# Performance work log

Hardware: AMD Instinct MI355X
Metric: run time of the kernel (lower is better)

The kernel has to match this reference:

```python
import jax, jax.numpy as jnp
import numpy as np

B, S, H, NH = 4, 4096, 1024, 16
D = H // NH
SCALE = 1.0 / float(np.sqrt(D))


def setup_inputs() -> dict:
    key = jax.random.key(0)
    ks = jax.random.split(key, 4)
    w = 0.02
    return {
        "hidden_states": jax.random.normal(ks[0], (B, S, H), jnp.float32),
        "attention_mask": jnp.zeros((B, 1, 1, S), jnp.float32),
        "Wq": jax.random.normal(ks[1], (H, H), jnp.float32) * w,
        "bq": jnp.zeros((H,), jnp.float32),
        "Wk": jax.random.normal(ks[2], (H, H), jnp.float32) * w,
        "bk": jnp.zeros((H,), jnp.float32),
        "Wv": jax.random.normal(ks[3], (H, H), jnp.float32) * w,
        "bv": jnp.zeros((H,), jnp.float32),
    }


def reference(hidden_states, attention_mask, Wq, bq, Wk, bk, Wv, bv):
    def heads(x):  # [B,S,H] -> [B,NH,S,D]
        return x.reshape(B, S, NH, D).transpose(0, 2, 1, 3)

    q = heads(hidden_states @ Wq.T + bq)
    k = heads(hidden_states @ Wk.T + bk)
    v = heads(hidden_states @ Wv.T + bv)

    # --- global token (position 0) attends to everything ---
    gq = q[:, :, 0:1]                                   # [B,NH,1,D]
    g_scores = jnp.einsum('bhqd,bhkd->bhqk', gq, k) * SCALE + attention_mask
    g_attn = jax.nn.softmax(g_scores, axis=-1)          # [B,NH,1,S]
    g_out = jnp.einsum('bhqk,bhkd->bhqd', g_attn, v)    # [B,NH,1,D]

    # --- local tokens: 2-way attention over {own key, global key} ---
    lq = q[:, :, 1:]                                    # [B,NH,S-1,D]
    s_self = jnp.einsum('bhsd,bhsd->bhs', lq, k[:, :, 1:]) * SCALE
    s_glob = jnp.einsum('bhsd,bhd->bhs', lq, k[:, :, 0]) * SCALE
    # order matches torch cat([own, global]) along the key axis
    l_attn = jax.nn.softmax(jnp.stack([s_self, s_glob], axis=-1), axis=-1)  # [B,NH,S-1,2]
    l_out = l_attn[..., 0:1] * v[:, :, 1:] + l_attn[..., 1:2] * v[:, :, 0:1]  # [B,NH,S-1,D]

    ctx = jnp.concatenate([g_out, l_out], axis=2)       # [B,NH,S,D]
    ctx = ctx.transpose(0, 2, 1, 3).reshape(B, S, H)
    # torch returns local_attentions with shape [B,NH,S-1,1,2]
    return ctx, l_attn[:, :, :, None, :]
```

## Files before the change

### kernel.cpp

```cpp
#include <hip/hip_runtime.h>
#include <cstdint>
#include <cstddef>

#define B_   4
#define S_   4096
#define H_   1024
#define NH_  16
#define D_   64
#define M_TOT (B_ * S_)
#define K_TOT H_
#define N_TOT (3 * H_)
#define SCALE_ 0.125f
#define NCH 4
#define CH (S_ / NCH)

typedef __bf16 bf16x8 __attribute__((ext_vector_type(8)));
typedef float  f32x4  __attribute__((ext_vector_type(4)));

__device__ __forceinline__ unsigned short f2b(float x) {
    unsigned int u = __float_as_uint(x);
    u += 0x7FFFu + ((u >> 16) & 1u);
    return (unsigned short)(u >> 16);
}
__device__ __forceinline__ float b2f(unsigned int u) {
    return __uint_as_float(u << 16);
}

__global__ __launch_bounds__(256) void cvt_x(const float* __restrict__ src,
                                             unsigned short* __restrict__ dst, int n4) {
    int i = blockIdx.x * blockDim.x + threadIdx.x;
    int stride = gridDim.x * blockDim.x;
    for (; i < n4; i += stride) {
        float4 v = ((const float4*)src)[i];
        ushort4 o;
        o.x = f2b(v.x); o.y = f2b(v.y); o.z = f2b(v.z); o.w = f2b(v.w);
        ((ushort4*)dst)[i] = o;
    }
}

__global__ __launch_bounds__(256) void cvt_w(const float* __restrict__ w0,
                                             const float* __restrict__ w1,
                                             const float* __restrict__ w2,
                                             unsigned short* __restrict__ dst) {
    const int per4 = H_ * H_ / 4;
    int i = blockIdx.x * blockDim.x + threadIdx.x;
    const float* s = (blockIdx.y == 0) ? w0 : (blockIdx.y == 1 ? w1 : w2);
    float4 v = ((const float4*)s)[i];
    ushort4 o;
    o.x = f2b(v.x); o.y = f2b(v.y); o.z = f2b(v.z); o.w = f2b(v.w);
    ((ushort4*)(dst + (size_t)blockIdx.y * H_ * H_))[i] = o;
}

__global__ __launch_bounds__(256) void gemm_qkv(const unsigned short* __restrict__ A,
                                                const unsigned short* __restrict__ W,
                                                const float* __restrict__ bq,
                                                const float* __restrict__ bk,
                                                const float* __restrict__ bv,
                                                unsigned short* __restrict__ C) {
    __shared__ unsigned short As[128 * 32] __attribute__((aligned(16)));
    __shared__ unsigned short Bs[128 * 32] __attribute__((aligned(16)));
    const int tid  = threadIdx.x;
    const int wid  = tid >> 6;
    const int lane = tid & 63;
    const int wm = wid >> 1, wn = wid & 1;
    const int m0 = blockIdx.y * 128;
    const int n0 = blockIdx.x * 128;

    f32x4 acc[4][4];
#pragma unroll
    for (int i = 0; i < 4; i++)
#pragma unroll
        for (int j = 0; j < 4; j++) acc[i][j] = (f32x4){0.f, 0.f, 0.f, 0.f};

    const int lrow = lane >> 2;
    const int lcol = (lane & 3) * 8;

    for (int k0 = 0; k0 < K_TOT; k0 += 32) {
#pragma unroll
        for (int i = 0; i < 2; i++) {
            const int r0 = wid * 32 + i * 16;
            const unsigned short* ga = A + (size_t)(m0 + r0 + lrow) * K_TOT + k0 + lcol;
            __builtin_amdgcn_global_load_lds(
                (const __attribute__((address_space(1))) void*)ga,
                (__attribute__((address_space(3))) void*)&As[r0 * 32], 16, 0, 0);
            const unsigned short* gb = W + (size_t)(n0 + r0 + lrow) * K_TOT + k0 + lcol;
            __builtin_amdgcn_global_load_lds(
                (const __attribute__((address_space(1))) void*)gb,
                (__attribute__((address_space(3))) void*)&Bs[r0 * 32], 16, 0, 0);
        }
        __syncthreads();

        bf16x8 af[4], bfv[4];
#pragma unroll
        for (int mi = 0; mi < 4; mi++)
            af[mi] = *(const bf16x8*)&As[(wm * 64 + mi * 16 + (lane & 15)) * 32 + (lane >> 4) * 8];
#pragma unroll
        for (int ni = 0; ni < 4; ni++)
            bfv[ni] = *(const bf16x8*)&Bs[(wn * 64 + ni * 16 + (lane & 15)) * 32 + (lane >> 4) * 8];
#pragma unroll
        for (int mi = 0; mi < 4; mi++)
#pragma unroll
            for (int ni = 0; ni < 4; ni++)
                acc[mi][ni] = __builtin_amdgcn_mfma_f32_16x16x32_bf16(af[mi], bfv[ni], acc[mi][ni], 0, 0, 0);
        __syncthreads();
    }

    const int col_l = lane & 15;
    const int quad  = lane >> 4;
#pragma unroll
    for (int mi = 0; mi < 4; mi++) {
#pragma unroll
        for (int ni = 0; ni < 4; ni++) {
            const int gc = n0 + wn * 64 + ni * 16 + col_l;
            const float bias = (gc < H_) ? bq[gc] : (gc < 2 * H_ ? bk[gc - H_] : bv[gc - 2 * H_]);
#pragma unroll
            for (int i = 0; i < 4; i++) {
                const int gr = m0 + wm * 64 + mi * 16 + quad * 4 + i;
                C[(size_t)gr * N_TOT + gc] = f2b(acc[mi][ni][i] + bias);
            }
        }
    }
}

__global__ __launch_bounds__(256) void gattn_part(const unsigned short* __restrict__ QKV,
                                                  const float* __restrict__ mask,
                                                  float* __restrict__ Pm,
                                                  float* __restrict__ Pl,
                                                  float* __restrict__ Po) {
    const int bh = blockIdx.x;
    const int b = bh >> 4, h = bh & 15;
    const int chunk = blockIdx.y;
    const int tid = threadIdx.x;
    const int w = tid >> 6, lane = tid & 63;

    __shared__ float gq_sh[D_];
    __shared__ float pr[CH];
    __shared__ float red[8];
    __shared__ float osum[4][D_];

    const unsigned short* gqp = QKV + (size_t)(b * S_) * N_TOT + h * D_;
    if (tid < D_) gq_sh[tid] = b2f(gqp[tid]);
    __syncthreads();

    const int s0 = chunk * CH;
    float sreg[4];
    float smax = -1e30f;
    for (int j = 0; j < 4; j++) {
        const int sl = tid + j * 256;
        const int s  = s0 + sl;
        const uint4* kp4 = (const uint4*)(QKV + (size_t)(b * S_ + s) * N_TOT + H_ + h * D_);
        float acc = 0.f;
#pragma unroll
        for (int c = 0; c < 8; c++) {
            uint4 r = kp4[c];
            acc += b2f(r.x & 0xffffu) * gq_sh[c * 8 + 0];
            acc += b2f(r.x >> 16)     * gq_sh[c * 8 + 1];
            acc += b2f(r.y & 0xffffu) * gq_sh[c * 8 + 2];
            acc += b2f(r.y >> 16)     * gq_sh[c * 8 + 3];
            acc += b2f(r.z & 0xffffu) * gq_sh[c * 8 + 4];
            acc += b2f(r.z >> 16)     * gq_sh[c * 8 + 5];
            acc += b2f(r.w & 0xffffu) * gq_sh[c * 8 + 6];
            acc += b2f(r.w >> 16)     * gq_sh[c * 8 + 7];
        }
        const float sv = acc * SCALE_ + mask[b * S_ + s];
        sreg[j] = sv;
        smax = fmaxf(smax, sv);
    }
    float wmax = smax;
#pragma unroll
    for (int m = 32; m >= 1; m >>= 1) wmax = fmaxf(wmax, __shfl_xor(wmax, m, 64));
    if (lane == 0) red[w] = wmax;
    __syncthreads();
    const float bmax = fmaxf(fmaxf(red[0], red[1]), fmaxf(red[2], red[3]));

    float lsum = 0.f;
    for (int j = 0; j < 4; j++) {
        const int sl = tid + j * 256;
        const float p = __expf(sreg[j] - bmax);
        pr[sl] = p;
        lsum += p;
    }
    float wsum = lsum;
#pragma unroll
    for (int m = 32; m >= 1; m >>= 1) wsum += __shfl_xor(wsum, m, 64);
    if (lane == 0) red[4 + w] = wsum;
    __syncthreads();
    const float bsum = red[4] + red[5] + red[6] + red[7];

    float o = 0.f;
    const int sbase = s0 + w * 256;
    for (int i = 0; i < 256; i++) {
        const int s = sbase + i;
        const float vv = b2f((unsigned int)QKV[(size_t)(b * S_ + s) * N_TOT + 2 * H_ + h * D_ + lane]);
        o += pr[w * 256 + i] * vv;
    }
    osum[w][lane] = o;
    __syncthreads();
    if (tid < D_) {
        const float ot = osum[0][tid] + osum[1][tid] + osum[2][tid] + osum[3][tid];
        Po[(size_t)(bh * NCH + chunk) * D_ + tid] = ot;
        if (tid == 0) {
            Pm[bh * NCH + chunk] = bmax;
            Pl[bh * NCH + chunk] = bsum;
        }
    }
}

__global__ __launch_bounds__(64) void gattn_comb(const float* __restrict__ Pm,
                                                 const float* __restrict__ Pl,
                                                 const float* __restrict__ Po,
                                                 float* __restrict__ out) {
    const int bh = blockIdx.x, d = threadIdx.x;
    const int b = bh >> 4, h = bh & 15;
    const float m0 = Pm[bh * 4 + 0], m1 = Pm[bh * 4 + 1], m2 = Pm[bh * 4 + 2], m3 = Pm[bh * 4 + 3];
    const float ms = fmaxf(fmaxf(m0, m1), fmaxf(m2, m3));
    const float e0 = __expf(m0 - ms), e1 = __expf(m1 - ms), e2 = __expf(m2 - ms), e3 = __expf(m3 - ms);
    const float z = Pl[bh * 4 + 0] * e0 + Pl[bh * 4 + 1] * e1 + Pl[bh * 4 + 2] * e2 + Pl[bh * 4 + 3] * e3;
    const float o = Po[(size_t)(bh * 4 + 0) * D_ + d] * e0 + Po[(size_t)(bh * 4 + 1) * D_ + d] * e1 +
                    Po[(size_t)(bh * 4 + 2) * D_ + d] * e2 + Po[(size_t)(bh * 4 + 3) * D_ + d] * e3;
    out[(size_t)b * S_ * H_ + (size_t)h * D_ + d] = o / z;
}

__global__ __launch_bounds__(256) void lattn(const unsigned short* __restrict__ QKV,
                                             float* __restrict__ ctx,
                                             float* __restrict__ lat) {
    const int bh = blockIdx.x;
    const int b = bh >> 4, h = bh & 15;
    const int w = threadIdx.x >> 6, lane = threadIdx.x & 63;
    const int s = 1 + blockIdx.y * 4 + w;
    if (s >= S_) return;

    const size_t rowS = (size_t)(b * S_ + s) * N_TOT + h * D_;
    const size_t row0 = (size_t)(b * S_) * N_TOT + h * D_;
    const float qd  = b2f((unsigned int)QKV[rowS + lane]);
    const float kd  = b2f((unsigned int)QKV[rowS + H_ + lane]);
    const float k0d = b2f((unsigned int)QKV[row0 + H_ + lane]);

    float ps = qd * kd, pg = qd * k0d;
#pragma unroll
    for (int m = 32; m >= 1; m >>= 1) {
        ps += __shfl_xor(ps, m, 64);
        pg += __shfl_xor(pg, m, 64);
    }
    ps *= SCALE_; pg *= SCALE_;
    const float mx = fmaxf(ps, pg);
    const float e0 = __expf(ps - mx), e1 = __expf(pg - mx);
    const float z = e0 + e1;
    const float p0 = e0 / z, p1 = e1 / z;

    const float vd  = b2f((unsigned int)QKV[rowS + 2 * H_ + lane]);
    const float v0d = b2f((unsigned int)QKV[row0 + 2 * H_ + lane]);
    ctx[(size_t)b * (S_ * H_) + (size_t)s * H_ + h * D_ + lane] = p0 * vd + p1 * v0d;
    if (lane == 0) {
        const size_t li = ((size_t)bh * (S_ - 1) + (s - 1)) * 2;
        lat[li]     = p0;
        lat[li + 1] = p1;
    }
}

extern "C" void kernel_launch(void* const* d_in, const int* in_sizes, int n_in,
                              void* d_out, int out_size, void* d_ws, size_t ws_size,
                              hipStream_t stream) {
    const float* hs   = (const float*)d_in[0];
    const float* mask = (const float*)d_in[1];
    const float* Wq   = (const float*)d_in[2];
    const float* bq   = (const float*)d_in[3];
    const float* Wk   = (const float*)d_in[4];
    const float* bk   = (const float*)d_in[5];
    const float* Wv   = (const float*)d_in[6];
    const float* bv   = (const float*)d_in[7];

    float* out = (float*)d_out;
    float* lat = out + (size_t)B_ * S_ * H_;

    char* ws = (char*)d_ws;
    const size_t offXb  = 0;
    const size_t offWb  = offXb  + (size_t)M_TOT * K_TOT * 2;
    const size_t offQKV = offWb  + (size_t)3 * H_ * H_ * 2;
    const size_t offPm  = offQKV + (size_t)M_TOT * N_TOT * 2;
    const size_t offPl  = offPm  + (size_t)B_ * NH_ * NCH * 4;
    const size_t offPo  = offPl  + (size_t)B_ * NH_ * NCH * 4;

    unsigned short* Xb  = (unsigned short*)(ws + offXb);
    unsigned short* Wb  = (unsigned short*)(ws + offWb);
    unsigned short* QKV = (unsigned short*)(ws + offQKV);
    float* Pm = (float*)(ws + offPm);
    float* Pl = (float*)(ws + offPl);
    float* Po = (float*)(ws + offPo);

    hipLaunchKernelGGL(cvt_x, dim3(4096), dim3(256), 0, stream, hs, Xb, M_TOT * K_TOT / 4);
    hipLaunchKernelGGL(cvt_w, dim3(H_ * H_ / 4 / 256, 3), dim3(256), 0, stream, Wq, Wk, Wv, Wb);
    hipLaunchKernelGGL(gemm_qkv, dim3(N_TOT / 128, M_TOT / 128), dim3(256), 0, stream,
                       Xb, Wb, bq, bk, bv, QKV);
    hipLaunchKernelGGL(gattn_part, dim3(B_ * NH_, NCH), dim3(256), 0, stream, QKV, mask, Pm, Pl, Po);
    hipLaunchKernelGGL(gattn_comb, dim3(B_ * NH_), dim3(64), 0, stream, Pm, Pl, Po, out);
    hipLaunchKernelGGL(lattn, dim3(B_ * NH_, 1024), dim3(256), 0, stream, QKV, out, lat);
}
```

Baseline: 346.2 us.

## Vectorize local attention, split global attention finer, merge conversion kernels

Fuses the input and weight bf16 conversion kernels into one launch. Increases the global-token attention split from 4 to 16 chunks so more blocks run with shorter serial V loops, and generalises the combine step accordingly. Rewrites local attention so each wave handles 8 rows with 16-byte vector loads and float4 stores instead of one row with scalar 2-byte accesses. This reduces launch overhead, improves occupancy and memory coalescing, at the cost of more partial results to combine.

```diff
diff --git a/kernel.cpp b/kernel.cpp
--- a/kernel.cpp
+++ b/kernel.cpp
@@ -11,7 +11,7 @@
 #define K_TOT H_
 #define N_TOT (3 * H_)
 #define SCALE_ 0.125f
-#define NCH 4
+#define NCH 16
 #define CH (S_ / NCH)
 
 typedef __bf16 bf16x8 __attribute__((ext_vector_type(8)));
@@ -25,30 +25,36 @@
 __device__ __forceinline__ float b2f(unsigned int u) {
     return __uint_as_float(u << 16);
 }
-
-__global__ __launch_bounds__(256) void cvt_x(const float* __restrict__ src,
-                                             unsigned short* __restrict__ dst, int n4) {
-    int i = blockIdx.x * blockDim.x + threadIdx.x;
-    int stride = gridDim.x * blockDim.x;
-    for (; i < n4; i += stride) {
-        float4 v = ((const float4*)src)[i];
-        ushort4 o;
+__device__ __forceinline__ void unp8(uint4 u, float* f) {
+    f[0] = b2f(u.x & 0xffffu); f[1] = b2f(u.x >> 16);
+    f[2] = b2f(u.y & 0xffffu); f[3] = b2f(u.y >> 16);
+    f[4] = b2f(u.z & 0xffffu); f[5] = b2f(u.z >> 16);
+    f[6] = b2f(u.w & 0xffffu); f[7] = b2f(u.w >> 16);
+}
+
+__global__ __launch_bounds__(256) void cvt_all(const float* __restrict__ hs,
+                                               const float* __restrict__ wq,
+                                               const float* __restrict__ wk,
+                                               const float* __restrict__ wv,
+                                               unsigned short* __restrict__ Xb,
+                                               unsigned short* __restrict__ Wb) {
+    const int i = blockIdx.x * 256 + threadIdx.x;
+    const int X4 = M_TOT * K_TOT / 4;
+    float4 v;
+    ushort4 o;
+    if (i < X4) {
+        v = ((const float4*)hs)[i];
         o.x = f2b(v.x); o.y = f2b(v.y); o.z = f2b(v.z); o.w = f2b(v.w);
-        ((ushort4*)dst)[i] = o;
-    }
-}
-
-__global__ __launch_bounds__(256) void cvt_w(const float* __restrict__ w0,
-                                             const float* __restrict__ w1,
-                                             const float* __restrict__ w2,
-                                             unsigned short* __restrict__ dst) {
-    const int per4 = H_ * H_ / 4;
-    int i = blockIdx.x * blockDim.x + threadIdx.x;
-    const float* s = (blockIdx.y == 0) ? w0 : (blockIdx.y == 1 ? w1 : w2);
-    float4 v = ((const float4*)s)[i];
-    ushort4 o;
-    o.x = f2b(v.x); o.y = f2b(v.y); o.z = f2b(v.z); o.w = f2b(v.w);
-    ((ushort4*)(dst + (size_t)blockIdx.y * H_ * H_))[i] = o;
+        ((ushort4*)Xb)[i] = o;
+    } else {
+        const int j = i - X4;
+        const int w = j >> 18;
+        const int off = j & 0x3ffff;
+        const float* s = (w == 0) ? wq : (w == 1 ? wk : wv);
+        v = ((const float4*)s)[off];
+        o.x = f2b(v.x); o.y = f2b(v.y); o.z = f2b(v.z); o.w = f2b(v.w);
+        ((ushort4*)(Wb + (size_t)w * H_ * H_))[off] = o;
+    }
 }
 
 __global__ __launch_bounds__(256) void gemm_qkv(const unsigned short* __restrict__ A,
@@ -143,44 +149,33 @@
     __syncthreads();
 
     const int s0 = chunk * CH;
-    float sreg[4];
-    float smax = -1e30f;
-    for (int j = 0; j < 4; j++) {
-        const int sl = tid + j * 256;
-        const int s  = s0 + sl;
-        const uint4* kp4 = (const uint4*)(QKV + (size_t)(b * S_ + s) * N_TOT + H_ + h * D_);
-        float acc = 0.f;
-#pragma unroll
-        for (int c = 0; c < 8; c++) {
-            uint4 r = kp4[c];
-            acc += b2f(r.x & 0xffffu) * gq_sh[c * 8 + 0];
-            acc += b2f(r.x >> 16)     * gq_sh[c * 8 + 1];
-            acc += b2f(r.y & 0xffffu) * gq_sh[c * 8 + 2];
-            acc += b2f(r.y >> 16)     * gq_sh[c * 8 + 3];
-            acc += b2f(r.z & 0xffffu) * gq_sh[c * 8 + 4];
-            acc += b2f(r.z >> 16)     * gq_sh[c * 8 + 5];
-            acc += b2f(r.w & 0xffffu) * gq_sh[c * 8 + 6];
-            acc += b2f(r.w >> 16)     * gq_sh[c * 8 + 7];
-        }
-        const float sv = acc * SCALE_ + mask[b * S_ + s];
-        sreg[j] = sv;
-        smax = fmaxf(smax, sv);
-    }
-    float wmax = smax;
+    const int s  = s0 + tid;
+    const uint4* kp4 = (const uint4*)(QKV + (size_t)(b * S_ + s) * N_TOT + H_ + h * D_);
+    float acc = 0.f;
+#pragma unroll
+    for (int c = 0; c < 8; c++) {
+        uint4 r = kp4[c];
+        acc += b2f(r.x & 0xffffu) * gq_sh[c * 8 + 0];
+        acc += b2f(r.x >> 16)     * gq_sh[c * 8 + 1];
+        acc += b2f(r.y & 0xffffu) * gq_sh[c * 8 + 2];
+        acc += b2f(r.y >> 16)     * gq_sh[c * 8 + 3];
+        acc += b2f(r.z & 0xffffu) * gq_sh[c * 8 + 4];
+        acc += b2f(r.z >> 16)     * gq_sh[c * 8 + 5];
+        acc += b2f(r.w & 0xffffu) * gq_sh[c * 8 + 6];
+        acc += b2f(r.w >> 16)     * gq_sh[c * 8 + 7];
+    }
+    const float sv = acc * SCALE_ + mask[b * S_ + s];
+
+    float wmax = sv;
 #pragma unroll
     for (int m = 32; m >= 1; m >>= 1) wmax = fmaxf(wmax, __shfl_xor(wmax, m, 64));
     if (lane == 0) red[w] = wmax;
     __syncthreads();
     const float bmax = fmaxf(fmaxf(red[0], red[1]), fmaxf(red[2], red[3]));
 
-    float lsum = 0.f;
-    for (int j = 0; j < 4; j++) {
-        const int sl = tid + j * 256;
-        const float p = __expf(sreg[j] - bmax);
-        pr[sl] = p;
-        lsum += p;
-    }
-    float wsum = lsum;
+    const float p = __expf(sv - bmax);
+    pr[tid] = p;
+    float wsum = p;
 #pragma unroll
     for (int m = 32; m >= 1; m >>= 1) wsum += __shfl_xor(wsum, m, 64);
     if (lane == 0) red[4 + w] = wsum;
@@ -188,11 +183,12 @@
     const float bsum = red[4] + red[5] + red[6] + red[7];
 
     float o = 0.f;
-    const int sbase = s0 + w * 256;
-    for (int i = 0; i < 256; i++) {
-        const int s = sbase + i;
-        const float vv = b2f((unsigned int)QKV[(size_t)(b * S_ + s) * N_TOT + 2 * H_ + h * D_ + lane]);
-        o += pr[w * 256 + i] * vv;
+    const int sbase = s0 + w * 64;
+#pragma unroll 8
+    for (int i = 0; i < 64; i++) {
+        const int si = sbase + i;
+        const float vv = b2f((unsigned int)QKV[(size_t)(b * S_ + si) * N_TOT + 2 * H_ + h * D_ + lane]);
+        o += pr[w * 64 + i] * vv;
     }
     osum[w][lane] = o;
     __syncthreads();
@@ -212,12 +208,16 @@
                                                  float* __restrict__ out) {
     const int bh = blockIdx.x, d = threadIdx.x;
     const int b = bh >> 4, h = bh & 15;
-    const float m0 = Pm[bh * 4 + 0], m1 = Pm[bh * 4 + 1], m2 = Pm[bh * 4 + 2], m3 = Pm[bh * 4 + 3];
-    const float ms = fmaxf(fmaxf(m0, m1), fmaxf(m2, m3));
-    const float e0 = __expf(m0 - ms), e1 = __expf(m1 - ms), e2 = __expf(m2 - ms), e3 = __expf(m3 - ms);
-    const float z = Pl[bh * 4 + 0] * e0 + Pl[bh * 4 + 1] * e1 + Pl[bh * 4 + 2] * e2 + Pl[bh * 4 + 3] * e3;
-    const float o = Po[(size_t)(bh * 4 + 0) * D_ + d] * e0 + Po[(size_t)(bh * 4 + 1) * D_ + d] * e1 +
-                    Po[(size_t)(bh * 4 + 2) * D_ + d] * e2 + Po[(size_t)(bh * 4 + 3) * D_ + d] * e3;
+    float ms = -1e30f;
+#pragma unroll
+    for (int c = 0; c < NCH; c++) ms = fmaxf(ms, Pm[bh * NCH + c]);
+    float z = 0.f, o = 0.f;
+#pragma unroll
+    for (int c = 0; c < NCH; c++) {
+        const float e = __expf(Pm[bh * NCH + c] - ms);
+        z += Pl[bh * NCH + c] * e;
+        o += Po[(size_t)(bh * NCH + c) * D_ + d] * e;
+    }
     out[(size_t)b * S_ * H_ + (size_t)h * D_ + d] = o / z;
 }
 
@@ -227,18 +227,25 @@
     const int bh = blockIdx.x;
     const int b = bh >> 4, h = bh & 15;
     const int w = threadIdx.x >> 6, lane = threadIdx.x & 63;
-    const int s = 1 + blockIdx.y * 4 + w;
+    const int g = lane >> 3;
+    const int l = lane & 7;
+    const int s = 1 + blockIdx.y * 32 + w * 8 + g;
     if (s >= S_) return;
 
-    const size_t rowS = (size_t)(b * S_ + s) * N_TOT + h * D_;
-    const size_t row0 = (size_t)(b * S_) * N_TOT + h * D_;
-    const float qd  = b2f((unsigned int)QKV[rowS + lane]);
-    const float kd  = b2f((unsigned int)QKV[rowS + H_ + lane]);
-    const float k0d = b2f((unsigned int)QKV[row0 + H_ + lane]);
-
-    float ps = qd * kd, pg = qd * k0d;
-#pragma unroll
-    for (int m = 32; m >= 1; m >>= 1) {
+    const size_t rowS = (size_t)(b * S_ + s) * N_TOT + h * D_ + l * 8;
+    const size_t row0 = (size_t)(b * S_) * N_TOT + h * D_ + l * 8;
+
+    uint4 qu  = *(const uint4*)(QKV + rowS);
+    uint4 ku  = *(const uint4*)(QKV + rowS + H_);
+    uint4 k0u = *(const uint4*)(QKV + row0 + H_);
+    float qf[8], kf[8], k0f[8];
+    unp8(qu, qf); unp8(ku, kf); unp8(k0u, k0f);
+
+    float ps = 0.f, pg = 0.f;
+#pragma unroll
+    for (int i = 0; i < 8; i++) { ps += qf[i] * kf[i]; pg += qf[i] * k0f[i]; }
+#pragma unroll
+    for (int m = 1; m < 8; m <<= 1) {
         ps += __shfl_xor(ps, m, 64);
         pg += __shfl_xor(pg, m, 64);
     }
@@ -248,13 +255,27 @@
     const float z = e0 + e1;
     const float p0 = e0 / z, p1 = e1 / z;
 
-    const float vd  = b2f((unsigned int)QKV[rowS + 2 * H_ + lane]);
-    const float v0d = b2f((unsigned int)QKV[row0 + 2 * H_ + lane]);
-    ctx[(size_t)b * (S_ * H_) + (size_t)s * H_ + h * D_ + lane] = p0 * vd + p1 * v0d;
-    if (lane == 0) {
-        const size_t li = ((size_t)bh * (S_ - 1) + (s - 1)) * 2;
-        lat[li]     = p0;
-        lat[li + 1] = p1;
+    uint4 vu  = *(const uint4*)(QKV + rowS + 2 * H_);
+    uint4 v0u = *(const uint4*)(QKV + row0 + 2 * H_);
+    float vf[8], v0f[8];
+    unp8(vu, vf); unp8(v0u, v0f);
+
+    float* cp = ctx + (size_t)b * (S_ * H_) + (size_t)s * H_ + h * D_ + l * 8;
+    float4 o0, o1;
+    o0.x = p0 * vf[0] + p1 * v0f[0];
+    o0.y = p0 * vf[1] + p1 * v0f[1];
+    o0.z = p0 * vf[2] + p1 * v0f[2];
+    o0.w = p0 * vf[3] + p1 * v0f[3];
+    o1.x = p0 * vf[4] + p1 * v0f[4];
+    o1.y = p0 * vf[5] + p1 * v0f[5];
+    o1.z = p0 * vf[6] + p1 * v0f[6];
+    o1.w = p0 * vf[7] + p1 * v0f[7];
+    ((float4*)cp)[0] = o0;
+    ((float4*)cp)[1] = o1;
+
+    if (l == 0) {
+        float2 lp; lp.x = p0; lp.y = p1;
+        ((float2*)(lat + ((size_t)bh * (S_ - 1) + (s - 1)) * 2))[0] = lp;
     }
 }
 
@@ -288,11 +309,12 @@
     float* Pl = (float*)(ws + offPl);
     float* Po = (float*)(ws + offPo);
 
-    hipLaunchKernelGGL(cvt_x, dim3(4096), dim3(256), 0, stream, hs, Xb, M_TOT * K_TOT / 4);
-    hipLaunchKernelGGL(cvt_w, dim3(H_ * H_ / 4 / 256, 3), dim3(256), 0, stream, Wq, Wk, Wv, Wb);
+    const int total4 = M_TOT * K_TOT / 4 + 3 * H_ * H_ / 4;
+    hipLaunchKernelGGL(cvt_all, dim3(total4 / 256), dim3(256), 0, stream,
+                       hs, Wq, Wk, Wv, Xb, Wb);
     hipLaunchKernelGGL(gemm_qkv, dim3(N_TOT / 128, M_TOT / 128), dim3(256), 0, stream,
                        Xb, Wb, bq, bk, bv, QKV);
     hipLaunchKernelGGL(gattn_part, dim3(B_ * NH_, NCH), dim3(256), 0, stream, QKV, mask, Pm, Pl, Po);
     hipLaunchKernelGGL(gattn_comb, dim3(B_ * NH_), dim3(64), 0, stream, Pm, Pl, Po, out);
-    hipLaunchKernelGGL(lattn, dim3(B_ * NH_, 1024), dim3(256), 0, stream, QKV, out, lat);
-}
+    hipLaunchKernelGGL(lattn, dim3(B_ * NH_, 128), dim3(256), 0, stream, QKV, out, lat);
+}
```

Result: faster. 308.8 us (-10.8%).
